# Performance work log

Hardware: AMD Instinct MI355X
Metric: run time of the kernel (lower is better)

## Reference

```python
import jax, jax.numpy as jnp
import numpy as np

BITS = 4
GROUP_SIZE = 128
IN_F = 4096
OUT_F = 11008
MAXQ = (1 << BITS) - 1
PACK = 32 // BITS  # 8 values per int32 word


def setup_inputs() -> dict:
    key = jax.random.key(0)
    k1, k2, k3, k4, k5 = jax.random.split(key, 5)
    x = jax.random.normal(k1, (2, 2048, IN_F), dtype=jnp.float32)
    qweight = jax.random.randint(k2, (IN_F // PACK, OUT_F), 0, 2147483647, dtype=jnp.int32)
    qzeros = jax.random.randint(k3, (IN_F // GROUP_SIZE, OUT_F // PACK), 0, 2147483647, dtype=jnp.int32)
    scales = jax.random.uniform(k4, (IN_F // GROUP_SIZE, OUT_F), dtype=jnp.float32) * 0.01 + 1e-4
    bias = jax.random.normal(k5, (OUT_F,), dtype=jnp.float32)
    return {"x": x, "qweight": qweight, "qzeros": qzeros, "scales": scales, "bias": bias}


def _dequant_weight(qweight, qzeros, scales):
    shifts = jnp.arange(0, 32, BITS, dtype=jnp.int32)
    # unpack packed int4 weights: [K/8, N] -> [K/8, 8, N] -> [K, N]
    w = (qweight[:, None, :] >> shifts[None, :, None]) & MAXQ
    w = w.reshape(-1, qweight.shape[-1]).astype(jnp.float32)  # [K, N]
    # unpack zero points: [G, N/8] -> [G, N/8, 8] -> [G, N]
    z = (qzeros[:, :, None] >> shifts[None, None, :]) & MAXQ
    z = z.reshape(qzeros.shape[0], -1).astype(jnp.float32)  # [G, N]
    gidx = jnp.arange(w.shape[0]) // GROUP_SIZE  # [K]
    # asymmetric group-wise dequant: (q - zero) * scale
    return (w - z[gidx]) * scales[gidx].astype(jnp.float32)  # [K, N]


def reference(x, qweight, qzeros, scales, bias):
    raw_dtype = x.dtype
    W = _dequant_weight(qweight, qzeros, scales)  # [K, N] fp32
    x2 = x.astype(jnp.float32).reshape(-1, x.shape[-1])  # [M, K]
    out = x2 @ W + bias.astype(jnp.float32)  # [M, N]
    return out.astype(raw_dtype).reshape(x.shape[:-1] + (W.shape[-1],))
```

## Files before the change

### kernel.cpp

```cpp
#include <hip/hip_runtime.h>
#include <hip/hip_bf16.h>
#include <stdint.h>

#define K_DIM 4096
#define N_DIM 11008
#define GROUP 128

typedef __attribute__((ext_vector_type(8))) __bf16 bf16x8;
typedef __attribute__((ext_vector_type(4))) float f32x4;
typedef __attribute__((address_space(3))) uint8_t lds_u8;
typedef __attribute__((address_space(3))) void lds_void;
typedef __attribute__((address_space(1))) const void g_void;

static __device__ inline __bf16 f2bf(float f) { return (__bf16)f; }

__global__ __launch_bounds__(256) void cvt_x_kernel(const float* __restrict__ x,
                                                    __bf16* __restrict__ xb, int total8) {
    int t = blockIdx.x * 256 + threadIdx.x;
    if (t >= total8) return;
    f32x4 a0 = *(const f32x4*)(x + (size_t)t * 8);
    f32x4 a1 = *(const f32x4*)(x + (size_t)t * 8 + 4);
    bf16x8 v;
    #pragma unroll
    for (int j = 0; j < 4; ++j) { v[j] = f2bf(a0[j]); v[j + 4] = f2bf(a1[j]); }
    *(bf16x8*)(xb + (size_t)t * 8) = v;
}

__global__ __launch_bounds__(256) void dequant_w_kernel(const int* __restrict__ qw,
                                                        const int* __restrict__ qz,
                                                        const float* __restrict__ sc,
                                                        __bf16* __restrict__ wb) {
    const int n   = blockIdx.x * 256 + threadIdx.x;
    const int kb0 = blockIdx.y * 8;
    const int g   = blockIdx.y >> 1;
    const float s   = sc[(size_t)g * N_DIM + n];
    const float nzs = -(float)((qz[(size_t)g * (N_DIM / 8) + (n >> 3)] >> ((n & 7) * 4)) & 15) * s;
    #pragma unroll
    for (int j = 0; j < 8; ++j) {
        const int w = qw[(size_t)(kb0 + j) * N_DIM + n];
        bf16x8 v;
        #pragma unroll
        for (int b = 0; b < 8; ++b)
            v[b] = f2bf(fmaf((float)((w >> (4 * b)) & 15), s, nzs));
        *(bf16x8*)(wb + (size_t)n * K_DIM + (size_t)(kb0 + j) * 8) = v;
    }
}

#define BM2 128
#define BN2 128
#define BK2 64
#define NT  (K_DIM / BK2)

__global__ __launch_bounds__(256, 2) void gemm128_kernel(
    const __bf16* __restrict__ xb, const __bf16* __restrict__ wb,
    const float* __restrict__ bias, float* __restrict__ out)
{
    __shared__ __align__(16) __bf16 As[2][BM2 * BK2];
    __shared__ __align__(16) __bf16 Bs[2][BN2 * BK2];

    const int tid  = threadIdx.x;
    const int lane = tid & 63;
    const int wid  = tid >> 6;
    const int wm = (wid >> 1) * 64;
    const int wn = (wid & 1) * 64;

    const int bid = blockIdx.x;
    const int wg  = (bid & 7) * 344 + (bid >> 3);
    const int m0 = (wg / 86) * BM2;
    const int n0 = (wg % 86) * BN2;

    const __bf16* pa[4];
    const __bf16* pb[4];
    int chk[4];
    #pragma unroll
    for (int l = 0; l < 4; ++l) {
        const int ch  = l * 256 + tid;
        const int row = ch >> 3;
        const int g   = (ch & 7) ^ (row & 7);
        chk[l] = ch;
        pa[l] = xb + (size_t)(m0 + row) * K_DIM + g * 8;
        pb[l] = wb + (size_t)(n0 + row) * K_DIM + g * 8;
    }
    lds_u8* baseA = (lds_u8*)&As[0][0];
    lds_u8* baseB = (lds_u8*)&Bs[0][0];

    auto STAGE = [&](int buf, int kofs) {
        lds_u8* dA_ = baseA + buf * (BM2 * BK2 * 2);
        lds_u8* dB_ = baseB + buf * (BN2 * BK2 * 2);
        #pragma unroll
        for (int l = 0; l < 4; ++l)
            __builtin_amdgcn_global_load_lds((g_void*)(pa[l] + kofs),
                                             (lds_void*)(dA_ + chk[l] * 16), 16, 0, 0);
        #pragma unroll
        for (int l = 0; l < 4; ++l)
            __builtin_amdgcn_global_load_lds((g_void*)(pb[l] + kofs),
                                             (lds_void*)(dB_ + chk[l] * 16), 16, 0, 0);
    };

    const int fr  = lane & 15;
    const int fc  = lane >> 4;
    const int swz = fr & 7;
    const int col0 = (fc ^ swz) * 8;
    const int col1 = ((4 + fc) ^ swz) * 8;
    const int rowoffA = (wm + fr) * BK2;
    const int rowoffB = (wn + fr) * BK2;

    f32x4 acc[4][4];
    #pragma unroll
    for (int m = 0; m < 4; ++m)
        #pragma unroll
        for (int n = 0; n < 4; ++n) acc[m][n] = (f32x4){0.f, 0.f, 0.f, 0.f};

    STAGE(0, 0);
    STAGE(1, BK2);
    asm volatile("s_waitcnt vmcnt(8)" ::: "memory");
    __builtin_amdgcn_sched_barrier(0);
    __builtin_amdgcn_s_barrier();
    __builtin_amdgcn_sched_barrier(0);

    for (int t = 0; t < NT; ++t) {
        const int cur = t & 1;
        const __bf16* ra = &As[0][0] + cur * (BM2 * BK2) + rowoffA;
        const __bf16* rb = &Bs[0][0] + cur * (BN2 * BK2) + rowoffB;
        bf16x8 aR[4], bR[8], a2[4];

        #pragma unroll
        for (int n = 0; n < 4; ++n) {
            bR[n * 2 + 0] = *(const bf16x8*)(rb + n * 1024 + col0);
            bR[n * 2 + 1] = *(const bf16x8*)(rb + n * 1024 + col1);
        }
        #pragma unroll
        for (int m = 0; m < 2; ++m) {
            aR[m * 2 + 0] = *(const bf16x8*)(ra + m * 1024 + col0);
            aR[m * 2 + 1] = *(const bf16x8*)(ra + m * 1024 + col1);
        }
        __builtin_amdgcn_s_setprio(1);
        #pragma unroll
        for (int m = 0; m < 2; ++m)
            #pragma unroll
            for (int n = 0; n < 4; ++n)
                #pragma unroll
                for (int kk = 0; kk < 2; ++kk)
                    acc[m][n] = __builtin_amdgcn_mfma_f32_16x16x32_bf16(
                        aR[m * 2 + kk], bR[n * 2 + kk], acc[m][n], 0, 0, 0);
        __builtin_amdgcn_s_setprio(0);

        #pragma unroll
        for (int m = 0; m < 2; ++m) {
            a2[m * 2 + 0] = *(const bf16x8*)(ra + (m + 2) * 1024 + col0);
            a2[m * 2 + 1] = *(const bf16x8*)(ra + (m + 2) * 1024 + col1);
        }
        asm volatile("s_waitcnt lgkmcnt(0)" ::: "memory");
        __builtin_amdgcn_sched_barrier(0);
        __builtin_amdgcn_s_barrier();
        __builtin_amdgcn_sched_barrier(0);
        if (t + 2 < NT) STAGE(cur, (t + 2) * BK2);

        __builtin_amdgcn_s_setprio(1);
        #pragma unroll
        for (int m = 0; m < 2; ++m)
            #pragma unroll
            for (int n = 0; n < 4; ++n)
                #pragma unroll
                for (int kk = 0; kk < 2; ++kk)
                    acc[m + 2][n] = __builtin_amdgcn_mfma_f32_16x16x32_bf16(
                        a2[m * 2 + kk], bR[n * 2 + kk], acc[m + 2][n], 0, 0, 0);
        __builtin_amdgcn_s_setprio(0);

        if (t + 2 < NT) { asm volatile("s_waitcnt vmcnt(8)" ::: "memory"); }
        else            { asm volatile("s_waitcnt vmcnt(0)" ::: "memory"); }
        __builtin_amdgcn_sched_barrier(0);
        __builtin_amdgcn_s_barrier();
        __builtin_amdgcn_sched_barrier(0);
    }

    const int cn  = lane & 15;
    const int cr4 = (lane >> 4) * 4;
    #pragma unroll
    for (int n = 0; n < 4; ++n) {
        const int col = n0 + wn + n * 16 + cn;
        const float bv = bias[col];
        #pragma unroll
        for (int m = 0; m < 4; ++m) {
            const int row = m0 + wm + m * 16 + cr4;
            #pragma unroll
            for (int r = 0; r < 4; ++r)
                out[(size_t)(row + r) * N_DIM + col] = acc[m][n][r] + bv;
        }
    }
}

#define FBM 128
#define FBN 128
#define FBK 32
#define FLDSS 40
__global__ __launch_bounds__(256) void gptq_gemm_fused_kernel(
    const float* __restrict__ x, const int* __restrict__ qw, const int* __restrict__ qz,
    const float* __restrict__ sc, const float* __restrict__ bias, float* __restrict__ out)
{
    __shared__ __align__(16) __bf16 Asm[FBM][FLDSS];
    __shared__ __align__(16) __bf16 Bsm[FBN][FLDSS];
    const int tid = threadIdx.x, lane = tid & 63, wid = tid >> 6;
    const int m0 = blockIdx.y * FBM, n0 = blockIdx.x * FBN;
    const int wm = (wid >> 1) * 64, wn = (wid & 1) * 64;
    f32x4 acc[4][4];
    #pragma unroll
    for (int i = 0; i < 4; ++i)
        #pragma unroll
        for (int j = 0; j < 4; ++j) acc[i][j] = (f32x4){0.f, 0.f, 0.f, 0.f};
    const int a_m = tid >> 2, a_h = tid & 3;
    const int b_n = tid & 127, b_k8 = tid >> 7;
    const int ng = n0 + b_n, zsh = (ng & 7) * 4;
    const int fr = lane & 15, fc = lane >> 4;
    for (int k0 = 0; k0 < K_DIM; k0 += FBK) {
        const int g = k0 >> 7;
        const float* xa = x + (size_t)(m0 + a_m) * K_DIM + k0 + a_h * 8;
        f32x4 a0 = *(const f32x4*)xa;
        f32x4 a1 = *(const f32x4*)(xa + 4);
        const float* xbp = xa + (size_t)64 * K_DIM;
        f32x4 a2 = *(const f32x4*)xbp;
        f32x4 a3 = *(const f32x4*)(xbp + 4);
        const int kb = (k0 >> 3) + b_k8;
        const int w0 = qw[(size_t)kb * N_DIM + ng];
        const int w1 = qw[(size_t)(kb + 2) * N_DIM + ng];
        const float s = sc[(size_t)g * N_DIM + ng];
        const float nzs = -(float)((qz[(size_t)g * (N_DIM / 8) + (ng >> 3)] >> zsh) & 15) * s;
        __syncthreads();
        bf16x8 av0, av1;
        #pragma unroll
        for (int j = 0; j < 4; ++j) {
            av0[j] = f2bf(a0[j]); av0[j + 4] = f2bf(a1[j]);
            av1[j] = f2bf(a2[j]); av1[j + 4] = f2bf(a3[j]);
        }
        *(bf16x8*)&Asm[a_m][a_h * 8] = av0;
        *(bf16x8*)&Asm[a_m + 64][a_h * 8] = av1;
        bf16x8 bv0, bv1;
        #pragma unroll
        for (int j = 0; j < 8; ++j) {
            bv0[j] = f2bf(fmaf((float)((w0 >> (4 * j)) & 15), s, nzs));
            bv1[j] = f2bf(fmaf((float)((w1 >> (4 * j)) & 15), s, nzs));
        }
        *(bf16x8*)&Bsm[b_n][b_k8 * 8] = bv0;
        *(bf16x8*)&Bsm[b_n][(b_k8 + 2) * 8] = bv1;
        __syncthreads();
        bf16x8 af[4], bfr[4];
        #pragma unroll
        for (int i = 0; i < 4; ++i) af[i] = *(const bf16x8*)&Asm[wm + i * 16 + fr][fc * 8];
        #pragma unroll
        for (int j = 0; j < 4; ++j) bfr[j] = *(const bf16x8*)&Bsm[wn + j * 16 + fr][fc * 8];
        #pragma unroll
        for (int i = 0; i < 4; ++i)
            #pragma unroll
            for (int j = 0; j < 4; ++j)
                acc[i][j] = __builtin_amdgcn_mfma_f32_16x16x32_bf16(af[i], bfr[j], acc[i][j], 0, 0, 0);
    }
    const int cn = lane & 15, cr4 = (lane >> 4) * 4;
    #pragma unroll
    for (int j = 0; j < 4; ++j) {
        const int col = n0 + wn + j * 16 + cn;
        const float bv = bias[col];
        #pragma unroll
        for (int i = 0; i < 4; ++i) {
            const int row = m0 + wm + i * 16 + cr4;
            #pragma unroll
            for (int r = 0; r < 4; ++r)
                out[(size_t)(row + r) * N_DIM + col] = acc[i][j][r] + bv;
        }
    }
}

extern "C" void kernel_launch(void* const* d_in, const int* in_sizes, int n_in,
                              void* d_out, int out_size, void* d_ws, size_t ws_size,
                              hipStream_t stream) {
    const float* x    = (const float*)d_in[0];
    const int*   qw   = (const int*)d_in[1];
    const int*   qz   = (const int*)d_in[2];
    const float* sc   = (const float*)d_in[3];
    const float* bias = (const float*)d_in[4];
    float* out = (float*)d_out;
    const int M = in_sizes[0] / K_DIM;

    const size_t xb_bytes = (size_t)M * K_DIM * sizeof(__bf16);
    const size_t wb_bytes = (size_t)N_DIM * K_DIM * sizeof(__bf16);
    if (ws_size >= xb_bytes + wb_bytes && (M % BM2) == 0) {
        __bf16* xb = (__bf16*)d_ws;
        __bf16* wb = (__bf16*)((uint8_t*)d_ws + xb_bytes);
        const int total8 = M * K_DIM / 8;
        cvt_x_kernel<<<dim3(total8 / 256), dim3(256), 0, stream>>>(x, xb, total8);
        dequant_w_kernel<<<dim3(N_DIM / 256, K_DIM / 8 / 8), dim3(256), 0, stream>>>(qw, qz, sc, wb);
        const int nblocks = (N_DIM / BN2) * (M / BM2);
        gemm128_kernel<<<dim3(nblocks), dim3(256), 0, stream>>>(xb, wb, bias, out);
    } else {
        gptq_gemm_fused_kernel<<<dim3(N_DIM / FBN, M / FBM), dim3(256), 0, stream>>>(x, qw, qz, sc, bias, out);
    }
}
```

Baseline: 516.1 us.

## Restructure bf16 GEMM to 512-thread 256x128 tiles with BK=32

```diff
diff --git a/kernel.cpp b/kernel.cpp
--- a/kernel.cpp
+++ b/kernel.cpp
@@ -46,12 +46,12 @@
     }
 }
 
-#define BM2 128
+#define BM2 256
 #define BN2 128
-#define BK2 64
+#define BK2 32
 #define NT  (K_DIM / BK2)
 
-__global__ __launch_bounds__(256, 2) void gemm128_kernel(
+__global__ __launch_bounds__(512, 4) void gemm_tlp_kernel(
     const __bf16* __restrict__ xb, const __bf16* __restrict__ wb,
     const float* __restrict__ bias, float* __restrict__ out)
 {
@@ -65,43 +65,37 @@
     const int wn = (wid & 1) * 64;
 
     const int bid = blockIdx.x;
-    const int wg  = (bid & 7) * 344 + (bid >> 3);
+    const int wg  = (bid & 7) * 172 + (bid >> 3);
     const int m0 = (wg / 86) * BM2;
     const int n0 = (wg % 86) * BN2;
 
-    const __bf16* pa[4];
-    const __bf16* pb[4];
-    int chk[4];
-    #pragma unroll
-    for (int l = 0; l < 4; ++l) {
-        const int ch  = l * 256 + tid;
-        const int row = ch >> 3;
-        const int g   = (ch & 7) ^ (row & 7);
-        chk[l] = ch;
-        pa[l] = xb + (size_t)(m0 + row) * K_DIM + g * 8;
-        pb[l] = wb + (size_t)(n0 + row) * K_DIM + g * 8;
-    }
+    const int chA0 = tid, chA1 = 512 + tid, chB = tid;
+    const int rA0 = chA0 >> 2, rA1 = chA1 >> 2, rB = chB >> 2;
+    const int gA0 = (chA0 & 3) ^ ((rA0 >> 1) & 3);
+    const int gA1 = (chA1 & 3) ^ ((rA1 >> 1) & 3);
+    const int gB  = (chB  & 3) ^ ((rB  >> 1) & 3);
+    const __bf16* pa0 = xb + (size_t)(m0 + rA0) * K_DIM + gA0 * 8;
+    const __bf16* pa1 = xb + (size_t)(m0 + rA1) * K_DIM + gA1 * 8;
+    const __bf16* pb0 = wb + (size_t)(n0 + rB)  * K_DIM + gB  * 8;
+
     lds_u8* baseA = (lds_u8*)&As[0][0];
     lds_u8* baseB = (lds_u8*)&Bs[0][0];
+    lds_u8* dA0 = baseA + chA0 * 16;
+    lds_u8* dA1 = baseA + chA1 * 16;
+    lds_u8* dB0 = baseB + chB  * 16;
 
     auto STAGE = [&](int buf, int kofs) {
-        lds_u8* dA_ = baseA + buf * (BM2 * BK2 * 2);
-        lds_u8* dB_ = baseB + buf * (BN2 * BK2 * 2);
-        #pragma unroll
-        for (int l = 0; l < 4; ++l)
-            __builtin_amdgcn_global_load_lds((g_void*)(pa[l] + kofs),
-                                             (lds_void*)(dA_ + chk[l] * 16), 16, 0, 0);
-        #pragma unroll
-        for (int l = 0; l < 4; ++l)
-            __builtin_amdgcn_global_load_lds((g_void*)(pb[l] + kofs),
-                                             (lds_void*)(dB_ + chk[l] * 16), 16, 0, 0);
+        const int oa = buf * (BM2 * BK2 * 2);
+        const int ob = buf * (BN2 * BK2 * 2);
+        __builtin_amdgcn_global_load_lds((g_void*)(pa0 + kofs), (lds_void*)(dA0 + oa), 16, 0, 0);
+        __builtin_amdgcn_global_load_lds((g_void*)(pa1 + kofs), (lds_void*)(dA1 + oa), 16, 0, 0);
+        __builtin_amdgcn_global_load_lds((g_void*)(pb0 + kofs), (lds_void*)(dB0 + ob), 16, 0, 0);
     };
 
     const int fr  = lane & 15;
     const int fc  = lane >> 4;
-    const int swz = fr & 7;
-    const int col0 = (fc ^ swz) * 8;
-    const int col1 = ((4 + fc) ^ swz) * 8;
+    const int swz = (fr >> 1) & 3;
+    const int col = (fc ^ swz) * 8;
     const int rowoffA = (wm + fr) * BK2;
     const int rowoffB = (wn + fr) * BK2;
 
@@ -113,7 +107,7 @@
 
     STAGE(0, 0);
     STAGE(1, BK2);
-    asm volatile("s_waitcnt vmcnt(8)" ::: "memory");
+    asm volatile("s_waitcnt vmcnt(3)" ::: "memory");
     __builtin_amdgcn_sched_barrier(0);
     __builtin_amdgcn_s_barrier();
     __builtin_amdgcn_sched_barrier(0);
@@ -122,34 +116,23 @@
         const int cur = t & 1;
         const __bf16* ra = &As[0][0] + cur * (BM2 * BK2) + rowoffA;
         const __bf16* rb = &Bs[0][0] + cur * (BN2 * BK2) + rowoffB;
-        bf16x8 aR[4], bR[8], a2[4];
-
-        #pragma unroll
-        for (int n = 0; n < 4; ++n) {
-            bR[n * 2 + 0] = *(const bf16x8*)(rb + n * 1024 + col0);
-            bR[n * 2 + 1] = *(const bf16x8*)(rb + n * 1024 + col1);
-        }
-        #pragma unroll
-        for (int m = 0; m < 2; ++m) {
-            aR[m * 2 + 0] = *(const bf16x8*)(ra + m * 1024 + col0);
-            aR[m * 2 + 1] = *(const bf16x8*)(ra + m * 1024 + col1);
-        }
+        bf16x8 aR[4], bR[4];
+
+        #pragma unroll
+        for (int n = 0; n < 4; ++n)
+            bR[n] = *(const bf16x8*)(rb + n * 512 + col);
+        #pragma unroll
+        for (int m = 0; m < 4; ++m)
+            aR[m] = *(const bf16x8*)(ra + m * 512 + col);
         __builtin_amdgcn_s_setprio(1);
         #pragma unroll
-        for (int m = 0; m < 2; ++m)
-            #pragma unroll
-            for (int n = 0; n < 4; ++n)
-                #pragma unroll
-                for (int kk = 0; kk < 2; ++kk)
-                    acc[m][n] = __builtin_amdgcn_mfma_f32_16x16x32_bf16(
-                        aR[m * 2 + kk], bR[n * 2 + kk], acc[m][n], 0, 0, 0);
+        for (int m = 0; m < 4; ++m)
+            #pragma unroll
+            for (int n = 0; n < 2; ++n)
+                acc[m][n] = __builtin_amdgcn_mfma_f32_16x16x32_bf16(
+                    aR[m], bR[n], acc[m][n], 0, 0, 0);
         __builtin_amdgcn_s_setprio(0);
 
-        #pragma unroll
-        for (int m = 0; m < 2; ++m) {
-            a2[m * 2 + 0] = *(const bf16x8*)(ra + (m + 2) * 1024 + col0);
-            a2[m * 2 + 1] = *(const bf16x8*)(ra + (m + 2) * 1024 + col1);
-        }
         asm volatile("s_waitcnt lgkmcnt(0)" ::: "memory");
         __builtin_amdgcn_sched_barrier(0);
         __builtin_amdgcn_s_barrier();
@@ -158,16 +141,14 @@
 
         __builtin_amdgcn_s_setprio(1);
         #pragma unroll
-        for (int m = 0; m < 2; ++m)
-            #pragma unroll
-            for (int n = 0; n < 4; ++n)
-                #pragma unroll
-                for (int kk = 0; kk < 2; ++kk)
-                    acc[m + 2][n] = __builtin_amdgcn_mfma_f32_16x16x32_bf16(
-                        a2[m * 2 + kk], bR[n * 2 + kk], acc[m + 2][n], 0, 0, 0);
+        for (int m = 0; m < 4; ++m)
+            #pragma unroll
+            for (int n = 2; n < 4; ++n)
+                acc[m][n] = __builtin_amdgcn_mfma_f32_16x16x32_bf16(
+                    aR[m], bR[n], acc[m][n], 0, 0, 0);
         __builtin_amdgcn_s_setprio(0);
 
-        if (t + 2 < NT) { asm volatile("s_waitcnt vmcnt(8)" ::: "memory"); }
+        if (t + 2 < NT) { asm volatile("s_waitcnt vmcnt(3)" ::: "memory"); }
         else            { asm volatile("s_waitcnt vmcnt(0)" ::: "memory"); }
         __builtin_amdgcn_sched_barrier(0);
         __builtin_amdgcn_s_barrier();
@@ -178,14 +159,14 @@
     const int cr4 = (lane >> 4) * 4;
     #pragma unroll
     for (int n = 0; n < 4; ++n) {
-        const int col = n0 + wn + n * 16 + cn;
-        const float bv = bias[col];
+        const int col_ = n0 + wn + n * 16 + cn;
+        const float bv = bias[col_];
         #pragma unroll
         for (int m = 0; m < 4; ++m) {
             const int row = m0 + wm + m * 16 + cr4;
             #pragma unroll
             for (int r = 0; r < 4; ++r)
-                out[(size_t)(row + r) * N_DIM + col] = acc[m][n][r] + bv;
+                out[(size_t)(row + r) * N_DIM + col_] = acc[m][n][r] + bv;
         }
     }
 }
@@ -289,7 +270,7 @@
         cvt_x_kernel<<<dim3(total8 / 256), dim3(256), 0, stream>>>(x, xb, total8);
         dequant_w_kernel<<<dim3(N_DIM / 256, K_DIM / 8 / 8), dim3(256), 0, stream>>>(qw, qz, sc, wb);
         const int nblocks = (N_DIM / BN2) * (M / BM2);
-        gemm128_kernel<<<dim3(nblocks), dim3(256), 0, stream>>>(xb, wb, bias, out);
+        gemm_tlp_kernel<<<dim3(nblocks), dim3(512), 0, stream>>>(xb, wb, bias, out);
     } else {
         gptq_gemm_fused_kernel<<<dim3(N_DIM / FBN, M / FBM), dim3(256), 0, stream>>>(x, qw, qz, sc, bias, out);
     }
```

Result: faster. 458.6 us (-11.1%).
